# Optimization experiments

Hardware: AMD Instinct MI355X
Metric: run time of the kernel (lower is better)

The kernel has to match this reference:

```python
import jax, jax.numpy as jnp
import numpy as np

D_NODE, C, N_HEAD = 64, 8, 8
LN_EPS = 1e-5
MASK_EPS = 1e-10
INF = 1e9


def setup_inputs() -> dict:
    key = jax.random.key(0)
    ks = jax.random.split(key, 12)
    B, S, R, D = 1, 2048, 384, D_NODE
    HC = N_HEAD * C
    M_raw = jax.random.normal(ks[0], (B, S, R, D), dtype=jnp.float32)
    M_mask = (jax.random.uniform(ks[1], (B, S, R)) > 0.1).astype(jnp.float32)
    sc = 1.0 / np.sqrt(D)
    return {
        "M_raw": M_raw,
        "M_mask": M_mask,
        "ln_g": jnp.ones((D,), jnp.float32),
        "ln_b": jnp.zeros((D,), jnp.float32),
        "Wq": jax.random.normal(ks[2], (D, HC), jnp.float32) * sc,
        "Wk": jax.random.normal(ks[3], (D, C), jnp.float32) * sc,
        "Wv": jax.random.normal(ks[4], (D, C), jnp.float32) * sc,
        "Wg": jax.random.normal(ks[5], (D, HC), jnp.float32) * sc,
        "bg": jnp.ones((HC,), jnp.float32),  # gating bias init to 1
        "Wo": jax.random.normal(ks[6], (HC, D), jnp.float32) * sc,
        "bo": jnp.zeros((D,), jnp.float32),
    }


def reference(M_raw, M_mask, ln_g, ln_b, Wq, Wk, Wv, Wg, bg, Wo, bo):
    # [B,S,R,D] -> [B,R,S,D]: attend over the sequence (column) axis per residue
    M = jnp.swapaxes(M_raw, -2, -3)
    mask = jnp.swapaxes(M_mask, -1, -2)  # [B,R,S]
    # LayerNorm over d_node
    mu = jnp.mean(M, axis=-1, keepdims=True)
    var = jnp.mean(jnp.square(M - mu), axis=-1, keepdims=True)
    M = (M - mu) * jax.lax.rsqrt(var + LN_EPS) * ln_g + ln_b
    # mean-pooled query over masked sequence positions -> [B,R,D]
    q_avg = jnp.sum(M * mask[..., None], axis=-2) / (jnp.sum(mask, axis=-1)[..., None] + MASK_EPS)
    q = (q_avg @ Wq).reshape(q_avg.shape[:-1] + (N_HEAD, C)) * (C ** -0.5)  # [B,R,H,c]
    k = M @ Wk  # [B,R,S,c] (shared across heads)
    v = M @ Wv  # [B,R,S,c]
    bias = (INF * (mask - 1.0))[..., None, :]  # [B,R,1,S]
    logits = jnp.einsum("brhc,brsc->brhs", q, k) + bias
    w = jax.nn.softmax(logits, axis=-1)
    o = jnp.einsum("brhs,brsc->brhc", w, v)  # [B,R,H,c]
    # per-position sigmoid gate broadcast against the single pooled output
    g = jax.nn.sigmoid(M @ Wg + bg).reshape(M.shape[:-1] + (N_HEAD, C))  # [B,R,S,H,c]
    go = (g * o[..., None, :, :]).reshape(M.shape[:-1] + (N_HEAD * C,))  # [B,R,S,H*c]
    out = go @ Wo + bo  # [B,R,S,D]
    return M_raw + jnp.swapaxes(out, -2, -3)
```

## Files before the change

kernel.cpp:

```cpp
#include <hip/hip_runtime.h>
#include <stdint.h>


#define DEV __device__ __forceinline__

typedef __attribute__((ext_vector_type(8))) short short8;
typedef __attribute__((ext_vector_type(4))) float floatx4;

static constexpr int S_DIM = 2048;
static constexpr int R_DIM = 384;
static constexpr int NCH   = 32;

static constexpr size_t KV_OFF    = 0;
static constexpr size_t QPART_OFF = 25165824;
static constexpr size_t O_OFF     = 28704768;

DEV float bf2f(uint32_t u) { union { uint32_t i; float f; } c; c.i = u << 16; return c.f; }
DEV uint16_t f2bf(float f) {
  union { float f; uint32_t i; } c; c.f = f;
  return (uint16_t)((c.i + 0x7FFFu + ((c.i >> 16) & 1u)) >> 16);
}
DEV void unpack8(uint4 w, float* x) {
  x[0] = bf2f(w.x & 0xffff); x[1] = bf2f(w.x >> 16);
  x[2] = bf2f(w.y & 0xffff); x[3] = bf2f(w.y >> 16);
  x[4] = bf2f(w.z & 0xffff); x[5] = bf2f(w.z >> 16);
  x[6] = bf2f(w.w & 0xffff); x[7] = bf2f(w.w >> 16);
}

__global__ __launch_bounds__(256) void k1_ln_kv(
    const float* __restrict__ M, const float* __restrict__ mask,
    const float* __restrict__ lng, const float* __restrict__ lnb,
    const float* __restrict__ Wk, const float* __restrict__ Wv,
    uint16_t* __restrict__ kv, float* __restrict__ qpart)
{
  __shared__ uint16_t WkvT[16 * 72];
  __shared__ uint16_t mlnA[4][16 * 72];
  __shared__ uint16_t kvS[4][4 * 64 * 16];

  const int tid = threadIdx.x;
  const int w = tid >> 6, lane = tid & 63;
  const int rl = lane >> 4, c4 = lane & 15;
  const int sc = blockIdx.x;
  const int s0 = sc * 64;
  const int r0w = blockIdx.y * 16 + w * 4;

#pragma unroll
  for (int i = 0; i < 4; ++i) {
    const int e = i * 256 + tid;
    const int n = e >> 6, d = e & 63;
    const float val = (n < 8) ? Wk[d * 8 + n] : Wv[d * 8 + (n - 8)];
    WkvT[n * 72 + d] = f2bf(val);
  }
  const float4 lngv = ((const float4*)lng)[c4];
  const float4 lnbv = ((const float4*)lnb)[c4];
  __syncthreads();

  const short8 b0 = *(const short8*)&WkvT[c4 * 72 + rl * 8];
  const short8 b1 = *(const short8*)&WkvT[c4 * 72 + 32 + rl * 8];

  uint16_t* mA = mlnA[w];
  uint16_t* kS = kvS[w];

  float qacc[4] = {0.f, 0.f, 0.f, 0.f};
  float cacc = 0.f;

#pragma unroll 2
  for (int grp = 0; grp < 16; ++grp) {
    const int sg = s0 + grp * 4;
    float4 xg[4];
    float mv[4];
#pragma unroll
    for (int si = 0; si < 4; ++si) {
      const size_t grow = (size_t)(sg + si) * R_DIM + r0w + rl;
      xg[si] = ((const float4*)(M + grow * 64))[c4];
      mv[si] = mask[grow];
    }
#pragma unroll
    for (int si = 0; si < 4; ++si) {
      const float4 x = xg[si];
      float sum = x.x + x.y + x.z + x.w;
      float ss = x.x * x.x + x.y * x.y + x.z * x.z + x.w * x.w;
#pragma unroll
      for (int off = 1; off < 16; off <<= 1) {
        sum += __shfl_xor(sum, off, 64);
        ss  += __shfl_xor(ss, off, 64);
      }
      const float mu = sum * (1.f / 64.f);
      const float var = ss * (1.f / 64.f) - mu * mu;
      const float rstd = 1.f / sqrtf(var + 1e-5f);
      float y[4];
      y[0] = (x.x - mu) * rstd * lngv.x + lnbv.x;
      y[1] = (x.y - mu) * rstd * lngv.y + lnbv.y;
      y[2] = (x.z - mu) * rstd * lngv.z + lnbv.z;
      y[3] = (x.w - mu) * rstd * lngv.w + lnbv.w;
      uint2 p;
      p.x = (uint32_t)f2bf(y[0]) | ((uint32_t)f2bf(y[1]) << 16);
      p.y = (uint32_t)f2bf(y[2]) | ((uint32_t)f2bf(y[3]) << 16);
      *(uint2*)&mA[(si * 4 + rl) * 72 + c4 * 4] = p;
      const float m = mv[si];
      qacc[0] += m * y[0]; qacc[1] += m * y[1];
      qacc[2] += m * y[2]; qacc[3] += m * y[3];
      cacc += m;
    }
    const short8 a0 = *(const short8*)&mA[c4 * 72 + rl * 8];
    const short8 a1 = *(const short8*)&mA[c4 * 72 + 32 + rl * 8];
    floatx4 c = {0.f, 0.f, 0.f, 0.f};
    c = __builtin_amdgcn_mfma_f32_16x16x32_bf16(a0, b0, c, 0, 0, 0);
    c = __builtin_amdgcn_mfma_f32_16x16x32_bf16(a1, b1, c, 0, 0, 0);
#pragma unroll
    for (int i = 0; i < 4; ++i)
      kS[i * 1024 + (grp * 4 + rl) * 16 + c4] = f2bf(c[i]);
  }

#pragma unroll
  for (int i = 0; i < 4; ++i) {
#pragma unroll
    for (int t = 0; t < 2; ++t) {
      const uint4 val = *(const uint4*)&kS[i * 1024 + t * 512 + lane * 8];
      *(uint4*)(kv + ((size_t)(r0w + i) * S_DIM + s0) * 16 + t * 512 + lane * 8) = val;
    }
  }
  *(float4*)&qpart[((size_t)(r0w + rl) * NCH + sc) * 72 + c4 * 4] =
      make_float4(qacc[0], qacc[1], qacc[2], qacc[3]);
  if (c4 == 0)
    qpart[((size_t)(r0w + rl) * NCH + sc) * 72 + 64] = cacc;
}

__global__ __launch_bounds__(256) void k2_attn(
    const float* __restrict__ Wq, const float* __restrict__ mask,
    const uint16_t* __restrict__ kv, const float* __restrict__ qpart,
    float* __restrict__ oG)
{
  __shared__ float qavgL[64], qLs[64];
  __shared__ float redmax[4][8], redden[4][8], redo[4][64];
  __shared__ float cntL;
  const int tid = threadIdx.x;
  const int r = blockIdx.x;
  const int lane = tid & 63, wv = tid >> 6;

  float qs = 0.f;
  if (tid < 65) {
#pragma unroll
    for (int c = 0; c < NCH; ++c) qs += qpart[((size_t)r * NCH + c) * 72 + tid];
    if (tid == 64) cntL = qs;
  }
  __syncthreads();
  if (tid < 64) qavgL[tid] = qs / (cntL + 1e-10f);
  __syncthreads();
  if (tid < 64) {
    float a = 0.f;
    for (int d = 0; d < 64; ++d) a += qavgL[d] * Wq[d * 64 + tid];
    qLs[tid] = a * 0.35355339059327373f;
  }
  __syncthreads();

  float l[64];
  float lm[8];
#pragma unroll
  for (int h = 0; h < 8; ++h) lm[h] = -3.0e38f;
  const uint4* kvp = (const uint4*)kv;
#pragma unroll
  for (int it = 0; it < 8; ++it) {
    const int s = it * 256 + tid;
    uint4 kw = kvp[((size_t)r * S_DIM + s) * 2];
    float k[8]; unpack8(kw, k);
    const float bias = (mask[(size_t)s * R_DIM + r] - 1.f) * 1e9f;
#pragma unroll
    for (int h = 0; h < 8; ++h) {
      float t = bias;
#pragma unroll
      for (int c = 0; c < 8; ++c) t += qLs[h * 8 + c] * k[c];
      l[it * 8 + h] = t;
      lm[h] = fmaxf(lm[h], t);
    }
  }
#pragma unroll
  for (int h = 0; h < 8; ++h)
#pragma unroll
    for (int off = 1; off < 64; off <<= 1) lm[h] = fmaxf(lm[h], __shfl_xor(lm[h], off, 64));
  if (lane == 0) {
#pragma unroll
    for (int h = 0; h < 8; ++h) redmax[wv][h] = lm[h];
  }
  __syncthreads();
  float gm[8];
#pragma unroll
  for (int h = 0; h < 8; ++h)
    gm[h] = fmaxf(fmaxf(redmax[0][h], redmax[1][h]), fmaxf(redmax[2][h], redmax[3][h]));

  float den[8], ao[64];
#pragma unroll
  for (int h = 0; h < 8; ++h) den[h] = 0.f;
#pragma unroll
  for (int i = 0; i < 64; ++i) ao[i] = 0.f;
#pragma unroll
  for (int it = 0; it < 8; ++it) {
    const int s = it * 256 + tid;
    uint4 vw = kvp[((size_t)r * S_DIM + s) * 2 + 1];
    float v[8]; unpack8(vw, v);
#pragma unroll
    for (int h = 0; h < 8; ++h) {
      const float w = __expf(l[it * 8 + h] - gm[h]);
      den[h] += w;
#pragma unroll
      for (int c = 0; c < 8; ++c) ao[h * 8 + c] += w * v[c];
    }
  }
#pragma unroll
  for (int st = 5; st >= 0; --st) {
    const int dist = 1 << st;
    const bool hi = (lane & dist) != 0;
#pragma unroll
    for (int j = 0; j < (1 << st); ++j) {
      const float send = hi ? ao[j] : ao[j + dist];
      const float recv = __shfl_xor(send, dist, 64);
      ao[j] = (hi ? ao[j + dist] : ao[j]) + recv;
    }
  }
#pragma unroll
  for (int h = 0; h < 8; ++h)
#pragma unroll
    for (int off = 1; off < 64; off <<= 1) den[h] += __shfl_xor(den[h], off, 64);

  redo[wv][lane] = ao[0];
  if (lane == 0) {
#pragma unroll
    for (int h = 0; h < 8; ++h) redden[wv][h] = den[h];
  }
  __syncthreads();
  if (tid < 64) {
    const float o = redo[0][tid] + redo[1][tid] + redo[2][tid] + redo[3][tid];
    const int h = tid >> 3;
    const float dd = redden[0][h] + redden[1][h] + redden[2][h] + redden[3][h];
    oG[(size_t)r * 64 + tid] = o / dd;
  }
}

__global__ __launch_bounds__(256, 2) void k3_out(
    const float* __restrict__ M, const float* __restrict__ oG,
    const float* __restrict__ Wg, const float* __restrict__ bg,
    const float* __restrict__ Wo, const float* __restrict__ bo,
    const float* __restrict__ lng, const float* __restrict__ lnb,
    float* __restrict__ out)
{
  __shared__ uint16_t WgT[64 * 72];
  __shared__ uint16_t WoT[64 * 72];
  __shared__ uint16_t mlnA[4][16 * 72];
  __shared__ uint16_t tA[4][16 * 72];

  const int tid = threadIdx.x;
  const int w = tid >> 6, lane = tid & 63;
  const int rl = lane >> 4, c4 = lane & 15;
  const int sc = blockIdx.x;
  const int s0 = sc * 64;
  const int r0w = blockIdx.y * 16 + w * 4;

#pragma unroll
  for (int i = 0; i < 16; ++i) {
    const int idx = i * 256 + tid;
    const int a = idx >> 6, b = idx & 63;
    WgT[b * 72 + a] = f2bf(Wg[idx]);
    WoT[b * 72 + a] = f2bf(Wo[idx]);
  }
  const float4 lngv = ((const float4*)lng)[c4];
  const float4 lnbv = ((const float4*)lnb)[c4];
  __syncthreads();

  short8 wgB[4][2], woB[4][2];
#pragma unroll
  for (int nt = 0; nt < 4; ++nt)
#pragma unroll
    for (int kk = 0; kk < 2; ++kk) {
      wgB[nt][kk] = *(const short8*)&WgT[(nt * 16 + c4) * 72 + kk * 32 + rl * 8];
      woB[nt][kk] = *(const short8*)&WoT[(nt * 16 + c4) * 72 + kk * 32 + rl * 8];
    }
  float og[4][4], bgr[4], bor[4];
#pragma unroll
  for (int nt = 0; nt < 4; ++nt) {
    bgr[nt] = bg[nt * 16 + c4];
    bor[nt] = bo[nt * 16 + c4];
#pragma unroll
    for (int i = 0; i < 4; ++i)
      og[nt][i] = oG[(size_t)(r0w + i) * 64 + nt * 16 + c4];
  }

  uint16_t* mA = mlnA[w];
  uint16_t* tAw = tA[w];

#pragma unroll 2
  for (int grp = 0; grp < 16; ++grp) {
    const int sg = s0 + grp * 4;
    float4 xg[4];
#pragma unroll
    for (int si = 0; si < 4; ++si)
      xg[si] = ((const float4*)(M + ((size_t)(sg + si) * R_DIM + r0w + rl) * 64))[c4];

#pragma unroll
    for (int si = 0; si < 4; ++si) {
      const float4 x = xg[si];
      float sum = x.x + x.y + x.z + x.w;
      float ss = x.x * x.x + x.y * x.y + x.z * x.z + x.w * x.w;
#pragma unroll
      for (int off = 1; off < 16; off <<= 1) {
        sum += __shfl_xor(sum, off, 64);
        ss  += __shfl_xor(ss, off, 64);
      }
      const float mu = sum * (1.f / 64.f);
      const float var = ss * (1.f / 64.f) - mu * mu;
      const float rstd = 1.f / sqrtf(var + 1e-5f);
      float y[4];
      y[0] = (x.x - mu) * rstd * lngv.x + lnbv.x;
      y[1] = (x.y - mu) * rstd * lngv.y + lnbv.y;
      y[2] = (x.z - mu) * rstd * lngv.z + lnbv.z;
      y[3] = (x.w - mu) * rstd * lngv.w + lnbv.w;
      uint2 p;
      p.x = (uint32_t)f2bf(y[0]) | ((uint32_t)f2bf(y[1]) << 16);
      p.y = (uint32_t)f2bf(y[2]) | ((uint32_t)f2bf(y[3]) << 16);
      *(uint2*)&mA[(si * 4 + rl) * 72 + c4 * 4] = p;
    }

    {
      const short8 a0 = *(const short8*)&mA[c4 * 72 + rl * 8];
      const short8 a1 = *(const short8*)&mA[c4 * 72 + 32 + rl * 8];
#pragma unroll
      for (int nt = 0; nt < 4; ++nt) {
        floatx4 c = {0.f, 0.f, 0.f, 0.f};
        c = __builtin_amdgcn_mfma_f32_16x16x32_bf16(a0, wgB[nt][0], c, 0, 0, 0);
        c = __builtin_amdgcn_mfma_f32_16x16x32_bf16(a1, wgB[nt][1], c, 0, 0, 0);
#pragma unroll
        for (int i = 0; i < 4; ++i) {
          const float z = c[i] + bgr[nt];
          const float gt = 1.0f / (1.0f + __expf(-z));
          tAw[(rl * 4 + i) * 72 + nt * 16 + c4] = f2bf(gt * og[nt][i]);
        }
      }
    }
    {
      const short8 a0 = *(const short8*)&tAw[c4 * 72 + rl * 8];
      const short8 a1 = *(const short8*)&tAw[c4 * 72 + 32 + rl * 8];
#pragma unroll
      for (int nt = 0; nt < 4; ++nt) {
        floatx4 c = {0.f, 0.f, 0.f, 0.f};
        c = __builtin_amdgcn_mfma_f32_16x16x32_bf16(a0, woB[nt][0], c, 0, 0, 0);
        c = __builtin_amdgcn_mfma_f32_16x16x32_bf16(a1, woB[nt][1], c, 0, 0, 0);
#pragma unroll
        for (int i = 0; i < 4; ++i)
          mA[(rl * 4 + i) * 72 + nt * 16 + c4] = f2bf(c[i] + bor[nt]);
      }
    }
#pragma unroll
    for (int si = 0; si < 4; ++si) {
      const uint2 tv = *(const uint2*)&mA[(si * 4 + rl) * 72 + c4 * 4];
      const float4 x = xg[si];
      float4 o;
      o.x = x.x + bf2f(tv.x & 0xffff);
      o.y = x.y + bf2f(tv.x >> 16);
      o.z = x.z + bf2f(tv.y & 0xffff);
      o.w = x.w + bf2f(tv.y >> 16);
      ((float4*)(out + ((size_t)(sg + si) * R_DIM + r0w + rl) * 64))[c4] = o;
    }
  }
}

extern "C" void kernel_launch(void* const* d_in, const int* in_sizes, int n_in,
                              void* d_out, int out_size, void* d_ws, size_t ws_size,
                              hipStream_t stream)
{
  const float* M    = (const float*)d_in[0];
  const float* mask = (const float*)d_in[1];
  const float* lng  = (const float*)d_in[2];
  const float* lnb  = (const float*)d_in[3];
  const float* Wq   = (const float*)d_in[4];
  const float* Wk   = (const float*)d_in[5];
  const float* Wv   = (const float*)d_in[6];
  const float* Wg   = (const float*)d_in[7];
  const float* bg   = (const float*)d_in[8];
  const float* Wo   = (const float*)d_in[9];
  const float* bo   = (const float*)d_in[10];
  float* out = (float*)d_out;

  char* ws = (char*)d_ws;
  uint16_t* kvB  = (uint16_t*)(ws + KV_OFF);
  float* qpartB  = (float*)(ws + QPART_OFF);
  float* oB      = (float*)(ws + O_OFF);

  k1_ln_kv<<<dim3(NCH, 24), 256, 0, stream>>>(M, mask, lng, lnb, Wk, Wv, kvB, qpartB);
  k2_attn<<<dim3(R_DIM), 256, 0, stream>>>(Wq, mask, kvB, qpartB, oB);
  k3_out<<<dim3(NCH, 24), 256, 0, stream>>>(M, oB, Wg, bg, Wo, bo, lng, lnb, out);
}
```

Baseline: 457.6 us.

## Fuse three kernels into one cooperative kernel with grid-wide syncs

```diff
diff --git a/kernel.cpp b/kernel.cpp
--- a/kernel.cpp
+++ b/kernel.cpp
@@ -1,8 +1,11 @@
 #include <hip/hip_runtime.h>
+#include <hip/hip_cooperative_groups.h>
 #include <stdint.h>
 
 
 #define DEV __device__ __forceinline__
+
+namespace cg = cooperative_groups;
 
 typedef __attribute__((ext_vector_type(8))) short short8;
 typedef __attribute__((ext_vector_type(4))) float floatx4;
@@ -27,6 +30,344 @@
   x[6] = bf2f(w.w & 0xffff); x[7] = bf2f(w.w >> 16);
 }
 
+__global__ __launch_bounds__(256, 3) void fused_all(
+    const float* __restrict__ M, const float* __restrict__ mask,
+    const float* __restrict__ lng, const float* __restrict__ lnb,
+    const float* __restrict__ Wq, const float* __restrict__ Wk,
+    const float* __restrict__ Wv, const float* __restrict__ Wg,
+    const float* __restrict__ bg, const float* __restrict__ Wo,
+    const float* __restrict__ bo, float* __restrict__ out,
+    uint16_t* __restrict__ kv, float* __restrict__ qpart, float* __restrict__ oG)
+{
+  __shared__ __align__(16) char smem[44288];
+  cg::grid_group grid = cg::this_grid();
+
+  const int tid = threadIdx.x;
+  const int w = tid >> 6, lane = tid & 63;
+  const int rl = lane >> 4, c4 = lane & 15;
+  const int sc = blockIdx.x;
+  const int s0 = sc * 64;
+  const int r0w = blockIdx.y * 16 + w * 4;
+
+  {
+    uint16_t* WkvT = (uint16_t*)smem;
+    uint16_t* mA   = (uint16_t*)(smem + 2304) + w * 1152;
+    uint16_t* kS   = (uint16_t*)(smem + 11520) + w * 4096;
+
+#pragma unroll
+    for (int i = 0; i < 4; ++i) {
+      const int e = i * 256 + tid;
+      const int n = e >> 6, d = e & 63;
+      const float val = (n < 8) ? Wk[d * 8 + n] : Wv[d * 8 + (n - 8)];
+      WkvT[n * 72 + d] = f2bf(val);
+    }
+    const float4 lngv = ((const float4*)lng)[c4];
+    const float4 lnbv = ((const float4*)lnb)[c4];
+    __syncthreads();
+
+    const short8 b0 = *(const short8*)&WkvT[c4 * 72 + rl * 8];
+    const short8 b1 = *(const short8*)&WkvT[c4 * 72 + 32 + rl * 8];
+
+    float qacc[4] = {0.f, 0.f, 0.f, 0.f};
+    float cacc = 0.f;
+
+#pragma unroll 2
+    for (int grp = 0; grp < 16; ++grp) {
+      const int sg = s0 + grp * 4;
+      float4 xg[4];
+      float mv[4];
+#pragma unroll
+      for (int si = 0; si < 4; ++si) {
+        const size_t grow = (size_t)(sg + si) * R_DIM + r0w + rl;
+        xg[si] = ((const float4*)(M + grow * 64))[c4];
+        mv[si] = mask[grow];
+      }
+#pragma unroll
+      for (int si = 0; si < 4; ++si) {
+        const float4 x = xg[si];
+        float sum = x.x + x.y + x.z + x.w;
+        float ss = x.x * x.x + x.y * x.y + x.z * x.z + x.w * x.w;
+#pragma unroll
+        for (int off = 1; off < 16; off <<= 1) {
+          sum += __shfl_xor(sum, off, 64);
+          ss  += __shfl_xor(ss, off, 64);
+        }
+        const float mu = sum * (1.f / 64.f);
+        const float var = ss * (1.f / 64.f) - mu * mu;
+        const float rstd = 1.f / sqrtf(var + 1e-5f);
+        float y[4];
+        y[0] = (x.x - mu) * rstd * lngv.x + lnbv.x;
+        y[1] = (x.y - mu) * rstd * lngv.y + lnbv.y;
+        y[2] = (x.z - mu) * rstd * lngv.z + lnbv.z;
+        y[3] = (x.w - mu) * rstd * lngv.w + lnbv.w;
+        uint2 p;
+        p.x = (uint32_t)f2bf(y[0]) | ((uint32_t)f2bf(y[1]) << 16);
+        p.y = (uint32_t)f2bf(y[2]) | ((uint32_t)f2bf(y[3]) << 16);
+        *(uint2*)&mA[(si * 4 + rl) * 72 + c4 * 4] = p;
+        const float m = mv[si];
+        qacc[0] += m * y[0]; qacc[1] += m * y[1];
+        qacc[2] += m * y[2]; qacc[3] += m * y[3];
+        cacc += m;
+      }
+      const short8 a0 = *(const short8*)&mA[c4 * 72 + rl * 8];
+      const short8 a1 = *(const short8*)&mA[c4 * 72 + 32 + rl * 8];
+      floatx4 c = {0.f, 0.f, 0.f, 0.f};
+      c = __builtin_amdgcn_mfma_f32_16x16x32_bf16(a0, b0, c, 0, 0, 0);
+      c = __builtin_amdgcn_mfma_f32_16x16x32_bf16(a1, b1, c, 0, 0, 0);
+#pragma unroll
+      for (int i = 0; i < 4; ++i)
+        kS[i * 1024 + (grp * 4 + rl) * 16 + c4] = f2bf(c[i]);
+    }
+
+#pragma unroll
+    for (int i = 0; i < 4; ++i) {
+#pragma unroll
+      for (int t = 0; t < 2; ++t) {
+        const uint4 val = *(const uint4*)&kS[i * 1024 + t * 512 + lane * 8];
+        *(uint4*)(kv + ((size_t)(r0w + i) * S_DIM + s0) * 16 + t * 512 + lane * 8) = val;
+      }
+    }
+    *(float4*)&qpart[((size_t)(r0w + rl) * NCH + sc) * 72 + c4 * 4] =
+        make_float4(qacc[0], qacc[1], qacc[2], qacc[3]);
+    if (c4 == 0)
+      qpart[((size_t)(r0w + rl) * NCH + sc) * 72 + 64] = cacc;
+  }
+
+  __threadfence();
+  grid.sync();
+
+  {
+    const int flat = blockIdx.y * NCH + blockIdx.x;
+    if (flat < R_DIM) {
+      const int r = flat;
+      float* qavgL  = (float*)smem;
+      float* qLs    = (float*)smem + 64;
+      float* redmax = (float*)smem + 128;
+      float* redden = (float*)smem + 160;
+      float* redo_  = (float*)smem + 192;
+      float* cntL   = (float*)smem + 448;
+      const int wv = w;
+
+      float qs = 0.f;
+      if (tid < 65) {
+#pragma unroll
+        for (int c = 0; c < NCH; ++c) qs += qpart[((size_t)r * NCH + c) * 72 + tid];
+        if (tid == 64) *cntL = qs;
+      }
+      __syncthreads();
+      if (tid < 64) qavgL[tid] = qs / (*cntL + 1e-10f);
+      __syncthreads();
+      if (tid < 64) {
+        float a = 0.f;
+        for (int d = 0; d < 64; ++d) a += qavgL[d] * Wq[d * 64 + tid];
+        qLs[tid] = a * 0.35355339059327373f;
+      }
+      __syncthreads();
+
+      const uint4* kvp = (const uint4*)kv;
+#pragma unroll
+      for (int hg = 0; hg < 2; ++hg) {
+        float l[32], lm[4];
+#pragma unroll
+        for (int h4 = 0; h4 < 4; ++h4) lm[h4] = -3.0e38f;
+#pragma unroll
+        for (int it = 0; it < 8; ++it) {
+          const int s = it * 256 + tid;
+          uint4 kw = kvp[((size_t)r * S_DIM + s) * 2];
+          float k[8]; unpack8(kw, k);
+          const float bias = (mask[(size_t)s * R_DIM + r] - 1.f) * 1e9f;
+#pragma unroll
+          for (int h4 = 0; h4 < 4; ++h4) {
+            const int h = hg * 4 + h4;
+            float t = bias;
+#pragma unroll
+            for (int c = 0; c < 8; ++c) t += qLs[h * 8 + c] * k[c];
+            l[it * 4 + h4] = t;
+            lm[h4] = fmaxf(lm[h4], t);
+          }
+        }
+#pragma unroll
+        for (int h4 = 0; h4 < 4; ++h4)
+#pragma unroll
+          for (int off = 1; off < 64; off <<= 1)
+            lm[h4] = fmaxf(lm[h4], __shfl_xor(lm[h4], off, 64));
+        if (lane == 0) {
+#pragma unroll
+          for (int h4 = 0; h4 < 4; ++h4) redmax[wv * 8 + hg * 4 + h4] = lm[h4];
+        }
+        __syncthreads();
+        float gm[4];
+#pragma unroll
+        for (int h4 = 0; h4 < 4; ++h4)
+          gm[h4] = fmaxf(fmaxf(redmax[0 * 8 + hg * 4 + h4], redmax[1 * 8 + hg * 4 + h4]),
+                         fmaxf(redmax[2 * 8 + hg * 4 + h4], redmax[3 * 8 + hg * 4 + h4]));
+
+        float den[4] = {0.f, 0.f, 0.f, 0.f};
+        float ao[32];
+#pragma unroll
+        for (int i = 0; i < 32; ++i) ao[i] = 0.f;
+#pragma unroll
+        for (int it = 0; it < 8; ++it) {
+          const int s = it * 256 + tid;
+          uint4 vw = kvp[((size_t)r * S_DIM + s) * 2 + 1];
+          float v[8]; unpack8(vw, v);
+#pragma unroll
+          for (int h4 = 0; h4 < 4; ++h4) {
+            const float wgt = __expf(l[it * 4 + h4] - gm[h4]);
+            den[h4] += wgt;
+#pragma unroll
+            for (int c = 0; c < 8; ++c) ao[h4 * 8 + c] += wgt * v[c];
+          }
+        }
+#pragma unroll
+        for (int st = 4; st >= 0; --st) {
+          const int dist = 1 << st;
+          const bool hi = (lane & dist) != 0;
+#pragma unroll
+          for (int j = 0; j < (1 << st); ++j) {
+            const float send = hi ? ao[j] : ao[j + dist];
+            const float recv = __shfl_xor(send, dist, 64);
+            ao[j] = (hi ? ao[j + dist] : ao[j]) + recv;
+          }
+        }
+        ao[0] += __shfl_xor(ao[0], 32, 64);
+#pragma unroll
+        for (int h4 = 0; h4 < 4; ++h4)
+#pragma unroll
+          for (int off = 1; off < 64; off <<= 1) den[h4] += __shfl_xor(den[h4], off, 64);
+
+        redo_[wv * 64 + hg * 32 + (lane & 31)] = ao[0];
+        if (lane == 0) {
+#pragma unroll
+          for (int h4 = 0; h4 < 4; ++h4) redden[wv * 8 + hg * 4 + h4] = den[h4];
+        }
+        __syncthreads();
+      }
+      if (tid < 64) {
+        const float o = redo_[0 * 64 + tid] + redo_[1 * 64 + tid] +
+                        redo_[2 * 64 + tid] + redo_[3 * 64 + tid];
+        const int h = tid >> 3;
+        const float dd = redden[0 * 8 + h] + redden[1 * 8 + h] +
+                         redden[2 * 8 + h] + redden[3 * 8 + h];
+        oG[(size_t)r * 64 + tid] = o / dd;
+      }
+    }
+  }
+
+  __threadfence();
+  grid.sync();
+
+  {
+    uint16_t* WgT = (uint16_t*)smem;
+    uint16_t* WoT = (uint16_t*)(smem + 9216);
+    uint16_t* mA  = (uint16_t*)(smem + 18432) + w * 1152;
+    uint16_t* tAw = (uint16_t*)(smem + 27648) + w * 1152;
+
+#pragma unroll
+    for (int i = 0; i < 16; ++i) {
+      const int idx = i * 256 + tid;
+      const int a = idx >> 6, b = idx & 63;
+      WgT[b * 72 + a] = f2bf(Wg[idx]);
+      WoT[b * 72 + a] = f2bf(Wo[idx]);
+    }
+    const float4 lngv = ((const float4*)lng)[c4];
+    const float4 lnbv = ((const float4*)lnb)[c4];
+    __syncthreads();
+
+    short8 wgB[4][2], woB[4][2];
+#pragma unroll
+    for (int nt = 0; nt < 4; ++nt)
+#pragma unroll
+      for (int kk = 0; kk < 2; ++kk) {
+        wgB[nt][kk] = *(const short8*)&WgT[(nt * 16 + c4) * 72 + kk * 32 + rl * 8];
+        woB[nt][kk] = *(const short8*)&WoT[(nt * 16 + c4) * 72 + kk * 32 + rl * 8];
+      }
+    float og[4][4], bgr[4], bor[4];
+#pragma unroll
+    for (int nt = 0; nt < 4; ++nt) {
+      bgr[nt] = bg[nt * 16 + c4];
+      bor[nt] = bo[nt * 16 + c4];
+#pragma unroll
+      for (int i = 0; i < 4; ++i)
+        og[nt][i] = oG[(size_t)(r0w + i) * 64 + nt * 16 + c4];
+    }
+
+#pragma unroll 2
+    for (int grp = 0; grp < 16; ++grp) {
+      const int sg = s0 + grp * 4;
+      float4 xg[4];
+#pragma unroll
+      for (int si = 0; si < 4; ++si)
+        xg[si] = ((const float4*)(M + ((size_t)(sg + si) * R_DIM + r0w + rl) * 64))[c4];
+
+#pragma unroll
+      for (int si = 0; si < 4; ++si) {
+        const float4 x = xg[si];
+        float sum = x.x + x.y + x.z + x.w;
+        float ss = x.x * x.x + x.y * x.y + x.z * x.z + x.w * x.w;
+#pragma unroll
+        for (int off = 1; off < 16; off <<= 1) {
+          sum += __shfl_xor(sum, off, 64);
+          ss  += __shfl_xor(ss, off, 64);
+        }
+        const float mu = sum * (1.f / 64.f);
+        const float var = ss * (1.f / 64.f) - mu * mu;
+        const float rstd = 1.f / sqrtf(var + 1e-5f);
+        float y[4];
+        y[0] = (x.x - mu) * rstd * lngv.x + lnbv.x;
+        y[1] = (x.y - mu) * rstd * lngv.y + lnbv.y;
+        y[2] = (x.z - mu) * rstd * lngv.z + lnbv.z;
+        y[3] = (x.w - mu) * rstd * lngv.w + lnbv.w;
+        uint2 p;
+        p.x = (uint32_t)f2bf(y[0]) | ((uint32_t)f2bf(y[1]) << 16);
+        p.y = (uint32_t)f2bf(y[2]) | ((uint32_t)f2bf(y[3]) << 16);
+        *(uint2*)&mA[(si * 4 + rl) * 72 + c4 * 4] = p;
+      }
+
+      {
+        const short8 a0 = *(const short8*)&mA[c4 * 72 + rl * 8];
+        const short8 a1 = *(const short8*)&mA[c4 * 72 + 32 + rl * 8];
+#pragma unroll
+        for (int nt = 0; nt < 4; ++nt) {
+          floatx4 c = {0.f, 0.f, 0.f, 0.f};
+          c = __builtin_amdgcn_mfma_f32_16x16x32_bf16(a0, wgB[nt][0], c, 0, 0, 0);
+          c = __builtin_amdgcn_mfma_f32_16x16x32_bf16(a1, wgB[nt][1], c, 0, 0, 0);
+#pragma unroll
+          for (int i = 0; i < 4; ++i) {
+            const float z = c[i] + bgr[nt];
+            const float gt = 1.0f / (1.0f + __expf(-z));
+            tAw[(rl * 4 + i) * 72 + nt * 16 + c4] = f2bf(gt * og[nt][i]);
+          }
+        }
+      }
+      {
+        const short8 a0 = *(const short8*)&tAw[c4 * 72 + rl * 8];
+        const short8 a1 = *(const short8*)&tAw[c4 * 72 + 32 + rl * 8];
+#pragma unroll
+        for (int nt = 0; nt < 4; ++nt) {
+          floatx4 c = {0.f, 0.f, 0.f, 0.f};
+          c = __builtin_amdgcn_mfma_f32_16x16x32_bf16(a0, woB[nt][0], c, 0, 0, 0);
+          c = __builtin_amdgcn_mfma_f32_16x16x32_bf16(a1, woB[nt][1], c, 0, 0, 0);
+#pragma unroll
+          for (int i = 0; i < 4; ++i)
+            mA[(rl * 4 + i) * 72 + nt * 16 + c4] = f2bf(c[i] + bor[nt]);
+        }
+      }
+#pragma unroll
+      for (int si = 0; si < 4; ++si) {
+        const uint2 tv = *(const uint2*)&mA[(si * 4 + rl) * 72 + c4 * 4];
+        const float4 x = xg[si];
+        float4 o;
+        o.x = x.x + bf2f(tv.x & 0xffff);
+        o.y = x.y + bf2f(tv.x >> 16);
+        o.z = x.z + bf2f(tv.y & 0xffff);
+        o.w = x.w + bf2f(tv.y >> 16);
+        ((float4*)(out + ((size_t)(sg + si) * R_DIM + r0w + rl) * 64))[c4] = o;
+      }
+    }
+  }
+}
+
 __global__ __launch_bounds__(256) void k1_ln_kv(
     const float* __restrict__ M, const float* __restrict__ mask,
     const float* __restrict__ lng, const float* __restrict__ lnb,
@@ -57,10 +398,8 @@
 
   const short8 b0 = *(const short8*)&WkvT[c4 * 72 + rl * 8];
   const short8 b1 = *(const short8*)&WkvT[c4 * 72 + 32 + rl * 8];
-
   uint16_t* mA = mlnA[w];
   uint16_t* kS = kvS[w];
-
   float qacc[4] = {0.f, 0.f, 0.f, 0.f};
   float cacc = 0.f;
 
@@ -283,7 +622,6 @@
     for (int i = 0; i < 4; ++i)
       og[nt][i] = oG[(size_t)(r0w + i) * 64 + nt * 16 + c4];
   }
-
   uint16_t* mA = mlnA[w];
   uint16_t* tAw = tA[w];
 
@@ -384,7 +722,26 @@
   float* qpartB  = (float*)(ws + QPART_OFF);
   float* oB      = (float*)(ws + O_OFF);
 
-  k1_ln_kv<<<dim3(NCH, 24), 256, 0, stream>>>(M, mask, lng, lnb, Wk, Wv, kvB, qpartB);
-  k2_attn<<<dim3(R_DIM), 256, 0, stream>>>(Wq, mask, kvB, qpartB, oB);
-  k3_out<<<dim3(NCH, 24), 256, 0, stream>>>(M, oB, Wg, bg, Wo, bo, lng, lnb, out);
+  static int coop_ok = -1;
+  if (coop_ok < 0) {
+    int v = 0;
+    if (hipDeviceGetAttribute(&v, hipDeviceAttributeCooperativeLaunch, 0) != hipSuccess) v = 0;
+    coop_ok = v;
+  }
+
+  bool launched = false;
+  if (coop_ok > 0) {
+    void* args[] = {(void*)&M, (void*)&mask, (void*)&lng, (void*)&lnb,
+                    (void*)&Wq, (void*)&Wk, (void*)&Wv, (void*)&Wg,
+                    (void*)&bg, (void*)&Wo, (void*)&bo, (void*)&out,
+                    (void*)&kvB, (void*)&qpartB, (void*)&oB};
+    hipError_t e = hipLaunchCooperativeKernel((const void*)fused_all, dim3(NCH, 24),
+                                              dim3(256, 1, 1), args, 0, stream);
+    launched = (e == hipSuccess);
+  }
+  if (!launched) {
+    k1_ln_kv<<<dim3(NCH, 24), 256, 0, stream>>>(M, mask, lng, lnb, Wk, Wv, kvB, qpartB);
+    k2_attn<<<dim3(R_DIM), 256, 0, stream>>>(Wq, mask, kvB, qpartB, oB);
+    k3_out<<<dim3(NCH, 24), 256, 0, stream>>>(M, oB, Wg, bg, Wo, bo, lng, lnb, out);
+  }
 }
```

Result: slower. 882.9 us (+93.0%).
